# Optimization experiments

Hardware: AMD Instinct MI355X
Metric: run time of the kernel (lower is better)

## Reference

```python
import jax, jax.numpy as jnp
import numpy as np

B, TE, TD, E, H, V, A, MAXOOV = 8, 400, 100, 128, 256, 50000, 612, 50
VEXT = V + MAXOOV


def setup_inputs():
    key = jax.random.key(0)
    it = iter(jax.random.split(key, 40))
    def nrm(shape, s=0.05):
        return jax.random.normal(next(it), shape, jnp.float32) * s
    inp = {
        "encoder_tokens": jax.random.randint(next(it), (B, TE), 0, V, dtype=jnp.int32),
        "decoder_tokens": jax.random.randint(next(it), (B, TD), 0, V, dtype=jnp.int32),
        "encoder_ext_tokens": jax.random.randint(next(it), (B, TE), 0, VEXT, dtype=jnp.int32),
        "encoder_mask": jnp.ones((B, TE), jnp.float32),
        "embedding": nrm((V, E)),
        "Wih_f": nrm((E, 4 * H)), "Whh_f": nrm((H, 4 * H)), "b_f": jnp.zeros((4 * H,), jnp.float32),
        "Wih_b": nrm((E, 4 * H)), "Whh_b": nrm((H, 4 * H)), "b_b": jnp.zeros((4 * H,), jnp.float32),
        "Wred": nrm((2 * H, H)), "bred": jnp.zeros((H,), jnp.float32),
        "Wenc_feat": nrm((2 * H, A)), "benc_feat": jnp.zeros((A,), jnp.float32),
        "v": nrm((A,), 1.0),
        "Wx": nrm((E + 2 * H, E)), "bx": jnp.zeros((E,), jnp.float32),
        "Wih_d": nrm((E, 4 * H)), "Whh_d": nrm((H, 4 * H)), "b_d": jnp.zeros((4 * H,), jnp.float32),
        "Wdf": nrm((TD, 2 * H, A)), "bdf": jnp.zeros((TD, A), jnp.float32),
        "Wpg": nrm((2 * H + H + H + E, 1)), "bpg": jnp.zeros((1,), jnp.float32),
        "Wout": nrm((H + 2 * H, H)), "bout": jnp.zeros((H,), jnp.float32),
        "Wv": nrm((H, V)), "bv": jnp.zeros((V,), jnp.float32),
    }
    return inp


def _lstm(xs, Wih, Whh, b):
    # xs: [T, B, E] -> outputs [T, B, H], final (h, c)
    def step(carry, x):
        h, c = carry
        g = x @ Wih + h @ Whh + b
        i, f, gg, o = jnp.split(g, 4, axis=-1)  # torch gate order i,f,g,o
        c = jax.nn.sigmoid(f) * c + jax.nn.sigmoid(i) * jnp.tanh(gg)
        h = jax.nn.sigmoid(o) * jnp.tanh(c)
        return (h, c), h
    z = jnp.zeros((xs.shape[1], Whh.shape[0]), xs.dtype)
    (hT, cT), hs = jax.lax.scan(step, (z, z), xs)
    return hs, hT, cT


def reference(encoder_tokens, decoder_tokens, encoder_ext_tokens, encoder_mask,
              embedding, Wih_f, Whh_f, b_f, Wih_b, Whh_b, b_b, Wred, bred,
              Wenc_feat, benc_feat, v, Wx, bx, Wih_d, Whh_d, b_d, Wdf, bdf,
              Wpg, bpg, Wout, bout, Wv, bv):
    # ---- bidirectional LSTM encoder (full-length sequences, mask == 1) ----
    enc_emb = embedding[encoder_tokens]               # [B, TE, E]
    xs = enc_emb.transpose(1, 0, 2)                   # [TE, B, E]
    hf, hTf, cTf = _lstm(xs, Wih_f, Whh_f, b_f)
    hb_rev, hTb, cTb = _lstm(xs[::-1], Wih_b, Whh_b, b_b)
    hb = hb_rev[::-1]
    enc_out = jnp.concatenate([hf, hb], -1).transpose(1, 0, 2)  # [B, TE, 2H]

    # ---- state reducer (original uses reduce_h_layer for BOTH h and c) ----
    h0 = jax.nn.relu(jnp.concatenate([hTf, hTb], -1) @ Wred + bred)
    c0 = jax.nn.relu(jnp.concatenate([cTf, cTb], -1) @ Wred + bred)

    # ---- 1x1 conv == linear on encoder states ----
    enc_feat = enc_out @ Wenc_feat + benc_feat        # [B, TE, A]

    dec_emb = embedding[decoder_tokens].transpose(1, 0, 2)  # [TD, B, E]

    def dec_step(carry, xs_t):
        h, c, ctx = carry
        emb_t, Wdf_t, bdf_t = xs_t
        x = jnp.concatenate([emb_t, ctx], -1) @ Wx + bx          # [B, E]
        g = x @ Wih_d + h @ Whh_d + b_d
        i, f, gg, o = jnp.split(g, 4, axis=-1)
        c = jax.nn.sigmoid(f) * c + jax.nn.sigmoid(i) * jnp.tanh(gg)
        h = jax.nn.sigmoid(o) * jnp.tanh(c)
        dec_feat = jnp.concatenate([h, c], -1) @ Wdf_t + bdf_t   # [B, A] (per-step weights)
        e = jnp.einsum('a,bta->bt', v, jnp.tanh(enc_feat + dec_feat[:, None, :]))
        attn = jax.nn.softmax(e, axis=-1) * encoder_mask
        attn = attn / attn.sum(-1, keepdims=True)
        ctx = jnp.einsum('bt,btd->bd', attn, enc_out)            # [B, 2H]
        p_gen = jax.nn.sigmoid(jnp.concatenate([ctx, h, c, x], -1) @ Wpg + bpg)  # [B, 1]
        out = jnp.concatenate([h, ctx], -1) @ Wout + bout        # [B, H]
        return (h, c, ctx), (out, attn, p_gen)

    ctx0 = jnp.zeros((enc_out.shape[0], 2 * H), enc_out.dtype)
    _, (outs, attns, pgens) = jax.lax.scan(dec_step, (h0, c0, ctx0), (dec_emb, Wdf, bdf))
    # outs [TD,B,H], attns [TD,B,TE], pgens [TD,B,1]

    # ---- pointer-generator mixture over extended vocab ----
    vocab_dist = jax.nn.softmax(outs @ Wv + bv, axis=-1)         # [TD, B, V]
    vocab_dist = pgens * vocab_dist
    attn_w = (1.0 - pgens) * attns                               # [TD, B, TE]

    def scatter_one(a, idx):
        return jnp.zeros((VEXT,), a.dtype).at[idx].add(a)
    copy_dist = jax.vmap(jax.vmap(scatter_one, in_axes=(0, 0)), in_axes=(0, None))(
        attn_w, encoder_ext_tokens)                              # [TD, B, VEXT]

    extra = jnp.zeros(vocab_dist.shape[:2] + (MAXOOV,), vocab_dist.dtype)
    final = jnp.concatenate([vocab_dist, extra], -1) + copy_dist # [TD, B, VEXT]
    return final
```

## Files before the change

### kernel.cpp

```cpp
#include <hip/hip_runtime.h>

#define DEVI __device__ __forceinline__

constexpr int B_ = 8, TE_ = 400, TD_ = 100, E_ = 128, H_ = 256;
constexpr int A_ = 612, V_ = 50000, VEXT_ = 50050;
constexpr int H4_ = 1024, H2_ = 512;
constexpr int NS_ = 16, SLW_ = 40;

constexpr size_t OFS_HBF  = 0;
constexpr size_t OFS_HBB  = 4096;
constexpr size_t OFS_CT   = 8192;
constexpr size_t OFS_CHC  = 12288;
constexpr size_t OFS_PG   = 32896;
constexpr size_t OFS_SROW = 33696;
constexpr size_t OFS_FLG  = 34496;
constexpr size_t OFS_ATT  = 35520;
constexpr size_t OFS_EO   = 355520;
constexpr size_t OFS_OUTS = OFS_EO;
constexpr size_t OFS_EF   = OFS_EO + (size_t)B_*TE_*H2_;

constexpr size_t DO_GDEC = 2ull*(size_t)TE_*B_*H4_;
constexpr size_t DO_XPRE = DO_GDEC + (size_t)TD_*B_*H4_;
constexpr size_t DO_CTXH = DO_XPRE + (size_t)TD_*B_*E_;
constexpr size_t DO_HCH  = DO_CTXH + (size_t)TD_*B_*H2_;
constexpr size_t DO_WCG  = DO_HCH + (size_t)TD_*B_*H2_;
constexpr size_t DO_EOWT = DO_WCG + (size_t)H2_*H4_;
constexpr size_t DO_EPB  = DO_EOWT + (size_t)B_*H4_*TE_;

#if defined(__has_builtin)
#if __has_builtin(__builtin_amdgcn_rcpf)
#define HAS_RCPF 1
#endif
#endif

DEVI float rcp_fast(float x) {
#ifdef HAS_RCPF
  return __builtin_amdgcn_rcpf(x);
#else
  return 1.0f / x;
#endif
}

DEVI float sigm(float x) { return rcp_fast(1.0f + __expf(-x)); }
DEVI float tanh_fast(float x) {
  float e = __expf(2.0f * x);
  return 1.0f - 2.0f * rcp_fast(e + 1.0f);
}

DEVI float ld_at(const float* p) {
  unsigned u = __hip_atomic_load((const unsigned*)p, __ATOMIC_RELAXED, __HIP_MEMORY_SCOPE_AGENT);
  return __uint_as_float(u);
}
DEVI void st_at(float* p, float v) {
  __hip_atomic_store((unsigned*)p, __float_as_uint(v), __ATOMIC_RELAXED, __HIP_MEMORY_SCOPE_AGENT);
}

#define WAIT_VM() do { asm volatile("s_waitcnt vmcnt(0)" ::: "memory"); \
                       __builtin_amdgcn_sched_barrier(0); } while (0)

DEVI float wave_max(float v) {
#pragma unroll
  for (int o = 32; o; o >>= 1) v = fmaxf(v, __shfl_xor(v, o));
  return v;
}
DEVI float wave_sum(float v) {
#pragma unroll
  for (int o = 32; o; o >>= 1) v += __shfl_xor(v, o);
  return v;
}

DEVI void flag_bar(unsigned* flags, int ncheck, int slot, unsigned ep, int stride) {
  __syncthreads();
  if (threadIdx.x == 0) {
    asm volatile("s_waitcnt vmcnt(0)" ::: "memory");
    __hip_atomic_store(&flags[slot * stride], ep, __ATOMIC_RELAXED, __HIP_MEMORY_SCOPE_AGENT);
  }
  if ((int)threadIdx.x < ncheck) {
    while (__hip_atomic_load(&flags[threadIdx.x * stride], __ATOMIC_RELAXED,
                             __HIP_MEMORY_SCOPE_AGENT) < ep) {
      __builtin_amdgcn_s_sleep(2);
    }
  }
  __syncthreads();
  asm volatile("" ::: "memory");
}

__global__ __launch_bounds__(256) void k0_wcg(
    const float* __restrict__ Wx, const float* __restrict__ Wih_d,
    float* __restrict__ dob, float* __restrict__ ws)
{
  __shared__ float AsT[32 * 64];
  __shared__ float Bsh[32 * 64];
  const float* Am = Wx + 128 * 128;
  float* C = dob + DO_WCG;
  const int ct = blockIdx.x, rt = blockIdx.y, tid = threadIdx.x;
  if (ct == 0 && rt == 0) {
    for (int i = tid; i < 8192; i += 256) ws[OFS_HBF + i] = 0.0f;
    unsigned* f = (unsigned*)(ws + OFS_FLG);
    for (int i = tid; i < 1024; i += 256) f[i] = 0u;
  }
  const int c0 = ct * 64, r0 = rt * 64;
  const int tx = tid & 15, ty = tid >> 4;
  float4 acc0 = make_float4(0,0,0,0), acc1 = acc0, acc2 = acc0, acc3 = acc0;
  for (int kc = 0; kc < 4; ++kc) {
#pragma unroll
    for (int i = 0; i < 2; ++i) {
      int q = tid * 2 + i;
      int r = q >> 3, kq = q & 7;
      float4 v = *(const float4*)&Am[(size_t)(r0 + r) * 128 + kc * 32 + kq * 4];
      AsT[(kq * 4 + 0) * 64 + r] = v.x; AsT[(kq * 4 + 1) * 64 + r] = v.y;
      AsT[(kq * 4 + 2) * 64 + r] = v.z; AsT[(kq * 4 + 3) * 64 + r] = v.w;
    }
#pragma unroll
    for (int i = 0; i < 2; ++i) {
      int q = tid * 2 + i;
      int kk = q >> 4, cq = q & 15;
      *(float4*)&Bsh[kk * 64 + cq * 4] =
          *(const float4*)&Wih_d[(size_t)(kc * 32 + kk) * H4_ + c0 + cq * 4];
    }
    __syncthreads();
#pragma unroll
    for (int kk = 0; kk < 32; ++kk) {
      float4 w4 = *(float4*)&Bsh[kk * 64 + tx * 4];
      const float* ar = &AsT[kk * 64 + ty * 4];
      acc0.x += ar[0]*w4.x; acc0.y += ar[0]*w4.y; acc0.z += ar[0]*w4.z; acc0.w += ar[0]*w4.w;
      acc1.x += ar[1]*w4.x; acc1.y += ar[1]*w4.y; acc1.z += ar[1]*w4.z; acc1.w += ar[1]*w4.w;
      acc2.x += ar[2]*w4.x; acc2.y += ar[2]*w4.y; acc2.z += ar[2]*w4.z; acc2.w += ar[2]*w4.w;
      acc3.x += ar[3]*w4.x; acc3.y += ar[3]*w4.y; acc3.z += ar[3]*w4.z; acc3.w += ar[3]*w4.w;
    }
    __syncthreads();
  }
  float4 r4[4] = {acc0, acc1, acc2, acc3};
#pragma unroll
  for (int i = 0; i < 4; ++i)
    *(float4*)&C[(size_t)(r0 + ty * 4 + i) * H4_ + c0 + tx * 4] = r4[i];
}

__global__ __launch_bounds__(256) void k1d_dec_pre(
    const int* __restrict__ dtok, const float* __restrict__ emb,
    const float* __restrict__ Wx, const float* __restrict__ bx,
    const float* __restrict__ Wih_d, const float* __restrict__ b_d,
    float* __restrict__ dob)
{
  __shared__ float er[8 * 128];
  __shared__ float xl[8 * 128];
  const int t = blockIdx.x, tid = threadIdx.x;
  for (int i = tid; i < 1024; i += 256) {
    int b = i >> 7, e = i & 127;
    er[i] = emb[(size_t)dtok[b * TD_ + t] * E_ + e];
  }
  __syncthreads();
  {
    const int col = tid & 127, bh = tid >> 7;
#pragma unroll
    for (int ii = 0; ii < 4; ++ii) {
      int b = bh + (ii << 1);
      float acc = bx[col];
      for (int k = 0; k < 128; ++k) acc += er[b * 128 + k] * Wx[(size_t)k * E_ + col];
      xl[b * 128 + col] = acc;
      dob[DO_XPRE + ((size_t)t * 8 + b) * E_ + col] = acc;
    }
  }
  __syncthreads();
  float bv[4];
#pragma unroll
  for (int g = 0; g < 4; ++g) bv[g] = b_d[g * H_ + tid];
  float af[32];
#pragma unroll
  for (int i = 0; i < 32; ++i) af[i] = bv[i & 3];
  for (int e = 0; e < E_; ++e) {
    float w[4];
#pragma unroll
    for (int g = 0; g < 4; ++g) w[g] = Wih_d[(size_t)e * H4_ + g * H_ + tid];
#pragma unroll
    for (int b = 0; b < 8; ++b) {
      float x = xl[b * 128 + e];
#pragma unroll
      for (int g = 0; g < 4; ++g) af[b * 4 + g] += x * w[g];
    }
  }
#pragma unroll
  for (int b = 0; b < 8; ++b)
#pragma unroll
    for (int g = 0; g < 4; ++g)
      dob[DO_GDEC + ((size_t)t * 8 + b) * H4_ + g * H_ + tid] = af[b * 4 + g];
}

__global__ __launch_bounds__(256, 1) void k2_encoder_scan(
    const int* __restrict__ etok, const float* __restrict__ emb,
    const float* __restrict__ Wih_f, const float* __restrict__ b_f,
    const float* __restrict__ Wih_b, const float* __restrict__ b_b,
    const float* __restrict__ Whh_f, const float* __restrict__ Whh_b,
    float* __restrict__ ws)
{
  __shared__ float sm[3072];
  __shared__ float part[2048];
  __shared__ int tokL[B_ * TE_];
  const int bid = blockIdx.x, tid = threadIdx.x;
  const int dir = bid >> 5, c0 = (bid & 31) * 8;
  const float* Whh = dir ? Whh_b : Whh_f;
  const float* Wih = dir ? Wih_b : Wih_f;
  const float* bbp = dir ? b_b : b_f;
  float* hb = ws + (dir ? OFS_HBB : OFS_HBF);
  float* cT = ws + OFS_CT;
  float* eo = ws + OFS_EO;
  unsigned* flg = (unsigned*)(ws + OFS_FLG) + (dir ? 128 : 0);
  const int slot = bid & 31;

  for (int i = tid; i < B_ * TE_; i += 256) tokL[i] = etok[i];

  const int jl = tid >> 3, kg = tid & 7;
  const int gt = jl >> 3, hcl = jl & 7;
  const int jcol = gt * H_ + c0 + hcl;
  float wreg[48];
#pragma unroll
  for (int kk = 0; kk < 48; ++kk) {
    if (kk < 32) wreg[kk] = Whh[(size_t)(kg + kk * 8) * H4_ + jcol];
    else         wreg[kk] = Wih[(size_t)(kg + (kk - 32) * 8) * H4_ + jcol];
  }
  const int uhc = tid >> 3, ub = tid & 7;
  float bias[4] = {0, 0, 0, 0};
  if (tid < 64) {
#pragma unroll
    for (int g = 0; g < 4; ++g) bias[g] = bbp[g * H_ + c0 + uhc];
  }
  const int ebb = tid >> 5, e4 = tid & 31;
  float c_reg = 0.0f;
  unsigned ep = 0;
  __syncthreads();

  for (int t = 0; t < TE_; ++t) {
    const int te = dir ? (TE_ - 1 - t) : t;
    float* hrd = hb + (t & 1) * 2048;
    float* hwr = hb + ((t & 1) ^ 1) * 2048;
    float4 ev = *(const float4*)&emb[(size_t)tokL[ebb * TE_ + te] * E_ + e4 * 4];
    float4 v0, v1;
    const float* a0p = &hrd[tid * 8];
    const float* a1p = &hrd[tid * 8 + 4];
    asm volatile(
        "global_load_dwordx4 %0, %2, off sc0 sc1\n\t"
        "global_load_dwordx4 %1, %3, off sc0 sc1"
        : "=&v"(v0), "=&v"(v1) : "v"(a0p), "v"(a1p));
    WAIT_VM();
    *(float4*)&sm[tid * 8] = v0;
    *(float4*)&sm[tid * 8 + 4] = v1;
    *(float4*)&sm[2048 + ebb * 128 + e4 * 4] = ev;
    __syncthreads();
    float acc[8] = {0, 0, 0, 0, 0, 0, 0, 0};
#pragma unroll
    for (int kk = 0; kk < 32; ++kk) {
      float w = wreg[kk];
      const float* hp = &sm[(kg + kk * 8) * 8];
#pragma unroll
      for (int b = 0; b < 8; ++b) acc[b] += hp[b] * w;
    }
#pragma unroll
    for (int kk = 32; kk < 48; ++kk) {
      float w = wreg[kk];
      const int e = kg + (kk - 32) * 8;
#pragma unroll
      for (int b = 0; b < 8; ++b) acc[b] += sm[2048 + b * 128 + e] * w;
    }
    *(float4*)&part[(jl * 8 + kg) * 8]     = make_float4(acc[0], acc[1], acc[2], acc[3]);
    *(float4*)&part[(jl * 8 + kg) * 8 + 4] = make_float4(acc[4], acc[5], acc[6], acc[7]);
    __syncthreads();
    if (tid < 64) {
      float g[4];
#pragma unroll
      for (int gg = 0; gg < 4; ++gg) {
        float s = bias[gg];
#pragma unroll
        for (int k2 = 0; k2 < 8; ++k2) s += part[((gg * 8 + uhc) * 8 + k2) * 8 + ub];
        g[gg] = s;
      }
      float ci = sigm(g[0]), cf = sigm(g[1]), cg = tanh_fast(g[2]), co = sigm(g[3]);
      c_reg = cf * c_reg + ci * cg;
      float hn = co * tanh_fast(c_reg);
      st_at(&hwr[(c0 + uhc) * 8 + ub], hn);
      eo[((size_t)ub * TE_ + te) * H2_ + dir * H_ + c0 + uhc] = hn;
      if (t == TE_ - 1) cT[ub * H2_ + dir * H_ + c0 + uhc] = c_reg;
    }
    ep++; flag_bar(flg, 32, slot, ep, 4);
  }
}

__global__ __launch_bounds__(256) void k3_encfeat(
    const float* __restrict__ eo, const float* __restrict__ Wef,
    const float* __restrict__ bef, float* __restrict__ ef)
{
  __shared__ float AsT[32 * 64];
  __shared__ float Wsh[32 * 64];
  const int ct = blockIdx.x, rt = blockIdx.y, tid = threadIdx.x;
  const int c0 = ct * 64, r0 = rt * 64;
  const int tx = tid & 15, ty = tid >> 4;
  float4 acc0 = make_float4(0,0,0,0), acc1 = acc0, acc2 = acc0, acc3 = acc0;
  for (int kc = 0; kc < 16; ++kc) {
#pragma unroll
    for (int i = 0; i < 2; ++i) {
      int q = tid * 2 + i;
      int r = q >> 3, kq = q & 7;
      float4 v = *(const float4*)&eo[(size_t)(r0 + r) * H2_ + kc * 32 + kq * 4];
      AsT[(kq * 4 + 0) * 64 + r] = v.x; AsT[(kq * 4 + 1) * 64 + r] = v.y;
      AsT[(kq * 4 + 2) * 64 + r] = v.z; AsT[(kq * 4 + 3) * 64 + r] = v.w;
    }
#pragma unroll
    for (int i = 0; i < 2; ++i) {
      int q = tid * 2 + i;
      int kk = q >> 4, cq = q & 15;
      int col = c0 + cq * 4;
      float4 v = make_float4(0,0,0,0);
      if (col < A_) v = *(const float4*)&Wef[(size_t)(kc * 32 + kk) * A_ + col];
      *(float4*)&Wsh[kk * 64 + cq * 4] = v;
    }
    __syncthreads();
#pragma unroll
    for (int kk = 0; kk < 32; ++kk) {
      float4 w4 = *(float4*)&Wsh[kk * 64 + tx * 4];
      const float* ar = &AsT[kk * 64 + ty * 4];
      acc0.x += ar[0]*w4.x; acc0.y += ar[0]*w4.y; acc0.z += ar[0]*w4.z; acc0.w += ar[0]*w4.w;
      acc1.x += ar[1]*w4.x; acc1.y += ar[1]*w4.y; acc1.z += ar[1]*w4.z; acc1.w += ar[1]*w4.w;
      acc2.x += ar[2]*w4.x; acc2.y += ar[2]*w4.y; acc2.z += ar[2]*w4.z; acc2.w += ar[2]*w4.w;
      acc3.x += ar[3]*w4.x; acc3.y += ar[3]*w4.y; acc3.z += ar[3]*w4.z; acc3.w += ar[3]*w4.w;
    }
    __syncthreads();
  }
  const int col = c0 + tx * 4;
  if (col < A_) {
    float4 bb = *(const float4*)&bef[col];
    float4 r4[4] = {acc0, acc1, acc2, acc3};
#pragma unroll
    for (int i = 0; i < 4; ++i) {
      int row = r0 + ty * 4 + i;
      float4 o = make_float4(r4[i].x + bb.x, r4[i].y + bb.y, r4[i].z + bb.z, r4[i].w + bb.w);
      *(float4*)&ef[(size_t)row * A_ + col] = o;
    }
  }
}

__global__ __launch_bounds__(256) void k3b_eowt(
    const float* __restrict__ eo, const float* __restrict__ dob_c, float* __restrict__ dob)
{
  __shared__ float Wt[32 * 64];
  __shared__ float Et[32 * 40];
  const float* Wcg = dob_c + DO_WCG;
  float* eoWT = dob + DO_EOWT;
  const int jt = blockIdx.x, tt = blockIdx.y, b = blockIdx.z, tid = threadIdx.x;
  const int j0 = jt * 64, te0 = tt * 40;
  const int j_l = tid & 63, tq = tid >> 6;
  float acc[10];
#pragma unroll
  for (int u = 0; u < 10; ++u) acc[u] = 0.0f;
  for (int kc = 0; kc < 16; ++kc) {
#pragma unroll
    for (int i = 0; i < 2; ++i) {
      int q = tid * 2 + i;
      int kk = q >> 4, j4 = q & 15;
      *(float4*)&Wt[kk * 64 + j4 * 4] =
          *(const float4*)&Wcg[(size_t)(kc * 32 + kk) * H4_ + j0 + j4 * 4];
    }
#pragma unroll
    for (int i = 0; i < 2; ++i) {
      int q = tid + i * 256;
      if (q < 320) {
        int te_l = q >> 3, kq = q & 7;
        float4 v = *(const float4*)&eo[((size_t)b * TE_ + te0 + te_l) * H2_ + kc * 32 + kq * 4];
        Et[(kq * 4 + 0) * 40 + te_l] = v.x; Et[(kq * 4 + 1) * 40 + te_l] = v.y;
        Et[(kq * 4 + 2) * 40 + te_l] = v.z; Et[(kq * 4 + 3) * 40 + te_l] = v.w;
      }
    }
    __syncthreads();
#pragma unroll
    for (int kk = 0; kk < 32; ++kk) {
      float w = Wt[kk * 64 + j_l];
      const float* ep2 = &Et[kk * 40 + tq * 10];
#pragma unroll
      for (int u = 0; u < 10; ++u) acc[u] += w * ep2[u];
    }
    __syncthreads();
  }
  float* outp = &eoWT[((size_t)b * H4_ + j0 + j_l) * TE_ + te0 + tq * 10];
#pragma unroll
  for (int u = 0; u < 10; ++u) outp[u] = acc[u];
}

__global__ __launch_bounds__(512, 1) void k4_decoder(
    const float* __restrict__ maskp,
    const float* __restrict__ Wred, const float* __restrict__ bred,
    const float* __restrict__ Whh_d,
    const float* __restrict__ Wdf, const float* __restrict__ bdf,
    const float* __restrict__ vvec, float* __restrict__ ws, float* __restrict__ dob)
{
  __shared__ float eoW[TE_ * 64];
  __shared__ float eu[TE_];
  __shared__ float hcL[512];
  __shared__ float red[16];
  __shared__ float gdL[64];
  __shared__ float gl[64];
  __shared__ float pgl[64 * 9];
  __shared__ float prt[1280];
  __shared__ float dfl[48];
  __shared__ float bdfL[48];
  __shared__ float vvL[48];

  float* chc = ws + OFS_CHC;
  float* att = ws + OFS_ATT;
  const float* efG = ws + OFS_EF;
  const float* hbf = ws + OFS_HBF;
  const float* hbb = ws + OFS_HBB;
  const float* cT  = ws + OFS_CT;
  unsigned* flgF = (unsigned*)(ws + OFS_FLG) + 256;
  const float* gdec = dob + DO_GDEC;
  const float* eoWT = dob + DO_EOWT;
  float* epb = dob + DO_EPB;
  float* hch = dob + DO_HCH;
  const int bid = blockIdx.x, tid = threadIdx.x;
  const int b = bid >> 4, s = bid & 15;
  unsigned* flgG = (unsigned*)(ws + OFS_FLG) + 512 + b * 64;
  const int a0 = s * SLW_, w = (s == 15) ? 12 : SLW_;
  const int nq = w >> 2;

  for (int i = tid; i < 64 * 100; i += 512) {
    int jgi = i / 100, c = i - jgi * 100;
    int jreal = (jgi >> 4) * 256 + s * 16 + (jgi & 15);
    float4 v = *(const float4*)&eoWT[((size_t)b * H4_ + jreal) * TE_ + c * 4];
    eoW[(c * 4 + 0) * 64 + jgi] = v.x;
    eoW[(c * 4 + 1) * 64 + jgi] = v.y;
    eoW[(c * 4 + 2) * 64 + jgi] = v.z;
    eoW[(c * 4 + 3) * 64 + jgi] = v.w;
  }
  const int jg = tid & 63, l8 = tid >> 6;
  const int jreal = (jg >> 4) * 256 + s * 16 + (jg & 15);
  float wreg[32];
#pragma unroll
  for (int kk = 0; kk < 32; ++kk)
    wreg[kk] = Whh_d[(size_t)(l8 + kk * 8) * H4_ + jreal];
  if (tid < w) vvL[tid] = vvec[a0 + tid];

  if (bid < 32) {
    const int isC = bid >> 4, pb = (bid >> 1) & 7, half = bid & 1;
    if (tid < 512)
      hcL[tid] = isC ? cT[pb * H2_ + tid]
                     : (tid < H_ ? hbf[tid * 8 + pb] : hbb[(tid - H_) * 8 + pb]);
    __syncthreads();
    {
      const int col_l = tid & 127, ks = tid >> 7;
      float acc = 0.0f;
      for (int kk = 0; kk < 128; ++kk) {
        int k = ks * 128 + kk;
        acc += hcL[k] * Wred[(size_t)k * H_ + half * 128 + col_l];
      }
      prt[ks * 128 + col_l] = acc;
    }
    __syncthreads();
    if (tid < 128) {
      float v2 = fmaxf(prt[tid] + prt[128 + tid] + prt[256 + tid] + prt[384 + tid] +
                       bred[half * 128 + tid], 0.0f);
      st_at(&chc[pb * H2_ + isC * H_ + half * 128 + tid], v2);
    }
  } else {
    float dm = 0.0f;
#pragma unroll
    for (int i = 0; i < 7; ++i) {
      int f = (bid - 32) * 3264 + i * 512 + tid;
      if (i * 512 + tid < 3264 && f < H2_ * A_) dm += Wdf[f];
    }
    asm volatile("" :: "v"(dm));
  }
  unsigned ep = 1;
  flag_bar(flgF, 128, bid, ep, 2);

  float c_reg = 0.0f;
  if (tid < 16) c_reg = ld_at(&chc[b * H2_ + H_ + s * 16 + tid]);
  unsigned epg = 0;

  for (int t = 0; t <= TD_; ++t) {
    const int cur = t & 1, nxt = cur ^ 1;

    {
      const int teA = (tid < TE_) ? tid : TE_ - 1;
      const int tcl = (t < TD_) ? t : TD_ - 1;
      const float* ae = &epb[((size_t)b * TE_ + teA) * 16];
      const float* ah = &chc[cur * 4096 + b * H2_ + (tid & 63) * 4];
      const int gi = tid & 15;
      const float* agd = &gdec[((size_t)tcl * 8 + b) * H4_ +
                               (gi >> 2) * 256 + s * 16 + (gi & 3) * 4];
      float4 v0, v1, v2, v3, vh, vgd;
      asm volatile(
          "global_load_dwordx4 %0, %6, off sc0 sc1\n\t"
          "global_load_dwordx4 %1, %7, off sc0 sc1\n\t"
          "global_load_dwordx4 %2, %8, off sc0 sc1\n\t"
          "global_load_dwordx4 %3, %9, off sc0 sc1\n\t"
          "global_load_dwordx4 %4, %10, off sc0 sc1\n\t"
          "global_load_dwordx4 %5, %11, off sc0 sc1"
          : "=&v"(v0), "=&v"(v1), "=&v"(v2), "=&v"(v3), "=&v"(vh), "=&v"(vgd)
          : "v"(ae), "v"(ae + 4), "v"(ae + 8), "v"(ae + 12), "v"(ah), "v"(agd));
      WAIT_VM();
      if (t > 0 && tid < TE_)
        eu[tid] = (v0.x + v0.y + v0.z + v0.w) + (v1.x + v1.y + v1.z + v1.w) +
                  (v2.x + v2.y + v2.z + v2.w) + (v3.x + v3.y + v3.z + v3.w);
      if (tid < 64) *(float4*)&hcL[tid * 4] = vh;
      if (tid < 16) *(float4*)&gdL[(gi >> 2) * 16 + (gi & 3) * 4] = vgd;
      __syncthreads();

      float inv = 0.0f;
      if (t > 0) {
        float m = (tid < TE_) ? eu[tid] : -3.4e38f;
        m = wave_max(m);
        if ((tid & 63) == 0) red[tid >> 6] = m;
        __syncthreads();
        m = red[0];
#pragma unroll
        for (int i = 1; i < 8; ++i) m = fmaxf(m, red[i]);
        float u = 0.0f;
        if (tid < TE_) {
          u = __expf(eu[tid] - m) * maskp[b * TE_ + tid];
          eu[tid] = u;
        }
        float sl = wave_sum(u);
        if ((tid & 63) == 0) red[8 + (tid >> 6)] = sl;
        __syncthreads();
        float S = 0.0f;
#pragma unroll
        for (int i = 0; i < 8; ++i) S += red[8 + i];
        inv = rcp_fast(S);
      }

      if (t > 0 && tid < 25)
        att[((size_t)(t - 1) * 8 + b) * TE_ + s * 25 + tid] = eu[s * 25 + tid] * inv;

      if (t < TD_) {
        float accG = 0.0f, accW = 0.0f;
        if (t > 0) {
          for (int te = l8; te < TE_; te += 8)
            accG += eoW[te * 64 + jg] * eu[te];
        }
#pragma unroll
        for (int kk = 0; kk < 32; ++kk)
          accW += wreg[kk] * hcL[l8 + kk * 8];
        pgl[jg * 9 + l8] = accG * inv + accW;
        __syncthreads();
        if (tid < 64) {
          float sg = gdL[tid];
#pragma unroll
          for (int l = 0; l < 8; ++l) sg += pgl[tid * 9 + l];
          gl[tid] = sg;
        }
        __syncthreads();
        if (tid < 16) {
          float g0 = gl[tid], g1 = gl[16 + tid], g2 = gl[32 + tid], g3 = gl[48 + tid];
          float ci = sigm(g0), cf = sigm(g1), cg = tanh_fast(g2), co = sigm(g3);
          c_reg = cf * c_reg + ci * cg;
          float hn = co * tanh_fast(c_reg);
          int hc = s * 16 + tid;
          st_at(&chc[nxt * 4096 + b * H2_ + hc], hn);
          st_at(&chc[nxt * 4096 + b * H2_ + H_ + hc], c_reg);
          hch[((size_t)t * 8 + b) * H2_ + hc] = hn;
          hch[((size_t)t * 8 + b) * H2_ + H_ + hc] = c_reg;
        }
      }
    }
    if (t == TD_) break;
    epg++; flag_bar(flgG, 16, s, epg, 4);

    {
      {
        const float* ahc = &chc[nxt * 4096 + b * H2_ + (tid & 127) * 4];
        const int cl = (tid < 10) ? tid : 9;
        const float* abf = &bdf[(size_t)t * A_ + a0 + cl * 4];
        float4 vhc, vbf;
        asm volatile(
            "global_load_dwordx4 %0, %2, off sc0 sc1\n\t"
            "global_load_dwordx4 %1, %3, off sc0 sc1"
            : "=&v"(vhc), "=&v"(vbf) : "v"(ahc), "v"(abf));
        WAIT_VM();
        if (tid < 128) *(float4*)&hcL[tid * 4] = vhc;
        if (tid < 10) *(float4*)&bdfL[tid * 4] = vbf;
      }
      __syncthreads();

      const float* wp = Wdf + (size_t)t * H2_ * A_;
      {
        const int kq = tid >> 4, al = tid & 15;
        if (al < nq) {
          float4 a4 = make_float4(0, 0, 0, 0);
          const float* wpc = wp + a0 + al * 4;
#pragma unroll
          for (int i = 0; i < 16; ++i) {
            int k = kq * 16 + i;
            float4 w4 = *(const float4*)&wpc[(size_t)k * A_];
            float hv = hcL[k];
            a4.x += hv * w4.x; a4.y += hv * w4.y; a4.z += hv * w4.z; a4.w += hv * w4.w;
          }
          *(float4*)&prt[(kq * 10 + al) * 4] = a4;
        }
      }
      float dm = 0.0f;
      if (t + 1 < TD_) {
        const float* wp1 = Wdf + (size_t)(t + 1) * H2_ * A_;
#pragma unroll
        for (int q = 0; q < 2; ++q) {
          int f = tid + q * 512;
          if (f < 640) {
            int r = f / 10, c4 = f - r * 10;
            if (c4 < nq) {
              float4 vx = *(const float4*)&wp1[(size_t)(b * 64 + r) * A_ + a0 + c4 * 4];
              dm += vx.x + vx.y + vx.z + vx.w;
            }
          }
        }
      }
      __syncthreads();
      if (tid < w) {
        float ssum = bdfL[tid];
        const int c4 = tid >> 2, r = tid & 3;
#pragma unroll
        for (int kq = 0; kq < 32; ++kq) ssum += prt[(kq * 10 + c4) * 4 + r];
        dfl[tid] = ssum;
      }
      __syncthreads();

      if (tid < TE_) {
        const float* efp = &efG[((size_t)b * TE_ + tid) * A_ + a0];
        float acc = 0.0f;
        for (int q = 0; q < nq; ++q) {
          float4 e4 = *(const float4*)&efp[q * 4];
          const float* dd = &dfl[q * 4];
          const float* vv = &vvL[q * 4];
          acc += vv[0] * tanh_fast(e4.x + dd[0]);
          acc += vv[1] * tanh_fast(e4.y + dd[1]);
          acc += vv[2] * tanh_fast(e4.z + dd[2]);
          acc += vv[3] * tanh_fast(e4.w + dd[3]);
        }
        st_at(&epb[((size_t)b * TE_ + tid) * 16 + s], acc);
      }
      asm volatile("" :: "v"(dm));
    }
    epg++; flag_bar(flgG, 16, s, epg, 4);
  }
}

__global__ __launch_bounds__(256) void k4c_ctx(
    const float* __restrict__ ws, float* __restrict__ dob)
{
  __shared__ float AsT[32 * 64];
  __shared__ float Bsh[32 * 64];
  const float* att = ws + OFS_ATT;
  const float* eo  = ws + OFS_EO;
  float* ctxh = dob + DO_CTXH;
  const int ct = blockIdx.x, rt = blockIdx.y, b = blockIdx.z, tid = threadIdx.x;
  const int c0 = ct * 64, r0 = rt * 64;
  const int tx = tid & 15, ty = tid >> 4;
  float4 acc0 = make_float4(0,0,0,0), acc1 = acc0, acc2 = acc0, acc3 = acc0;
  for (int kc = 0; kc < 13; ++kc) {
#pragma unroll
    for (int i = 0; i < 2; ++i) {
      int q = tid * 2 + i;
      int r = q >> 3, kq = q & 7;
      int k = kc * 32 + kq * 4;
      float4 v = make_float4(0, 0, 0, 0);
      if (k < TE_ && r0 + r < TD_)
        v = *(const float4*)&att[((size_t)(r0 + r) * 8 + b) * TE_ + k];
      AsT[(kq * 4 + 0) * 64 + r] = v.x; AsT[(kq * 4 + 1) * 64 + r] = v.y;
      AsT[(kq * 4 + 2) * 64 + r] = v.z; AsT[(kq * 4 + 3) * 64 + r] = v.w;
    }
#pragma unroll
    for (int i = 0; i < 2; ++i) {
      int q = tid * 2 + i;
      int kk = q >> 4, cq = q & 15;
      int k = kc * 32 + kk;
      float4 v = make_float4(0, 0, 0, 0);
      if (k < TE_) v = *(const float4*)&eo[((size_t)b * TE_ + k) * H2_ + c0 + cq * 4];
      *(float4*)&Bsh[kk * 64 + cq * 4] = v;
    }
    __syncthreads();
#pragma unroll
    for (int kk = 0; kk < 32; ++kk) {
      float4 w4 = *(float4*)&Bsh[kk * 64 + tx * 4];
      const float* ar = &AsT[kk * 64 + ty * 4];
      acc0.x += ar[0]*w4.x; acc0.y += ar[0]*w4.y; acc0.z += ar[0]*w4.z; acc0.w += ar[0]*w4.w;
      acc1.x += ar[1]*w4.x; acc1.y += ar[1]*w4.y; acc1.z += ar[1]*w4.z; acc1.w += ar[1]*w4.w;
      acc2.x += ar[2]*w4.x; acc2.y += ar[2]*w4.y; acc2.z += ar[2]*w4.z; acc2.w += ar[2]*w4.w;
      acc3.x += ar[3]*w4.x; acc3.y += ar[3]*w4.y; acc3.z += ar[3]*w4.z; acc3.w += ar[3]*w4.w;
    }
    __syncthreads();
  }
  float4 r4[4] = {acc0, acc1, acc2, acc3};
#pragma unroll
  for (int i = 0; i < 4; ++i) {
    int row = r0 + ty * 4 + i;
    if (row < TD_)
      *(float4*)&ctxh[((size_t)row * 8 + b) * H2_ + c0 + tx * 4] = r4[i];
  }
}

__global__ __launch_bounds__(256) void k4b_post(
    const float* __restrict__ Wx, const float* __restrict__ Wout, const float* __restrict__ bout,
    const float* __restrict__ Wpg, const float* __restrict__ bpg,
    float* __restrict__ ws, const float* __restrict__ dob)
{
  __shared__ float hcl[4096], ctxl[4096], cpl[4096], xl[1024], red2[256];
  const int t = blockIdx.x, tid = threadIdx.x;
  const float* hch  = dob + DO_HCH;
  const float* ctxh = dob + DO_CTXH;
  const float* xpre = dob + DO_XPRE;
  for (int i = tid; i < 4096; i += 256) {
    hcl[i]  = hch[(size_t)t * 4096 + i];
    ctxl[i] = ctxh[(size_t)t * 4096 + i];
    cpl[i]  = t ? ctxh[(size_t)(t - 1) * 4096 + i] : 0.0f;
  }
  __syncthreads();
  {
    const int col = tid & 127, bh = tid >> 7;
#pragma unroll
    for (int ii = 0; ii < 4; ++ii) {
      int b = bh + (ii << 1);
      float acc = xpre[(size_t)t * 1024 + b * E_ + col];
      for (int k = 0; k < H2_; ++k) acc += cpl[b * H2_ + k] * Wx[(size_t)(128 + k) * E_ + col];
      xl[b * E_ + col] = acc;
    }
  }
  __syncthreads();
  {
    const int col = tid;
    for (int b = 0; b < 8; ++b) {
      float acc = bout[col];
      for (int k = 0; k < 768; ++k)
        acc += (k < H_ ? hcl[b * H2_ + k] : ctxl[b * H2_ + (k - H_)]) * Wout[(size_t)k * H_ + col];
      ws[OFS_OUTS + ((size_t)t * 8 + b) * H_ + col] = acc;
    }
  }
  {
    const int b = tid >> 5, sg = tid & 31;
    float acc = 0.0f;
    for (int j = 0; j < 36; ++j) {
      int k = sg * 36 + j;
      float xv;
      if (k < H2_)       xv = ctxl[b * H2_ + k];
      else if (k < 768)  xv = hcl[b * H2_ + (k - H2_)];
      else if (k < 1024) xv = hcl[b * H2_ + H_ + (k - 768)];
      else               xv = xl[b * E_ + (k - 1024)];
      acc += xv * Wpg[k];
    }
    red2[tid] = acc;
    __syncthreads();
    if (tid < 8) {
      float s = 0.0f;
      for (int k2 = 0; k2 < 32; ++k2) s += red2[tid * 32 + k2];
      ws[OFS_PG + t * 8 + tid] = sigm(s + bpg[0]);
    }
  }
}

__global__ __launch_bounds__(256) void k5a_logits(
    const float* __restrict__ outs, const float* __restrict__ Wv,
    const float* __restrict__ bv, float* __restrict__ out)
{
  __shared__ float aT[32 * 64];
  __shared__ float wl[32 * 256];
  const int rt = blockIdx.x, ct = blockIdx.y, tid = threadIdx.x;
  const int r0 = rt * 64, c0 = ct * 256;
  const int cq = tid & 63, rg = tid >> 6;
  float4 acc[16];
#pragma unroll
  for (int i = 0; i < 16; ++i) acc[i] = make_float4(0, 0, 0, 0);
  for (int kc = 0; kc < 8; ++kc) {
#pragma unroll
    for (int i = 0; i < 2; ++i) {
      int q = tid * 2 + i;
      int r = q >> 3, kq = q & 7;
      float4 v = make_float4(0, 0, 0, 0);
      if (r0 + r < 800) v = *(const float4*)&outs[(size_t)(r0 + r) * H_ + kc * 32 + kq * 4];
      aT[(kq * 4 + 0) * 64 + r] = v.x; aT[(kq * 4 + 1) * 64 + r] = v.y;
      aT[(kq * 4 + 2) * 64 + r] = v.z; aT[(kq * 4 + 3) * 64 + r] = v.w;
    }
#pragma unroll
    for (int i = 0; i < 8; ++i) {
      int q = tid + i * 256;
      int kk = q >> 6, c4 = q & 63;
      int col = c0 + c4 * 4;
      float4 v = make_float4(0, 0, 0, 0);
      if (col < V_) v = *(const float4*)&Wv[(size_t)(kc * 32 + kk) * V_ + col];
      *(float4*)&wl[kk * 256 + c4 * 4] = v;
    }
    __syncthreads();
#pragma unroll
    for (int kk = 0; kk < 32; ++kk) {
      float4 w4 = *(float4*)&wl[kk * 256 + cq * 4];
      const float* ar = &aT[kk * 64 + rg * 16];
#pragma unroll
      for (int rr = 0; rr < 16; ++rr) {
        float a = ar[rr];
        acc[rr].x += a * w4.x; acc[rr].y += a * w4.y;
        acc[rr].z += a * w4.z; acc[rr].w += a * w4.w;
      }
    }
    __syncthreads();
  }
  const int col = c0 + cq * 4;
  if (col < V_) {
    float4 bb = *(const float4*)&bv[col];
#pragma unroll
    for (int rr = 0; rr < 16; ++rr) {
      int row = r0 + rg * 16 + rr;
      if (row < 800) {
        float2 lo = make_float2(acc[rr].x + bb.x, acc[rr].y + bb.y);
        float2 hi = make_float2(acc[rr].z + bb.z, acc[rr].w + bb.w);
        *(float2*)&out[(size_t)row * VEXT_ + col] = lo;
        *(float2*)&out[(size_t)row * VEXT_ + col + 2] = hi;
      }
    }
  }
}

__global__ __launch_bounds__(256) void k5b_rowsum(const float* __restrict__ out, float* __restrict__ Srow)
{
  __shared__ float red[256];
  const int r = blockIdx.x, tid = threadIdx.x;
  const float* base = out + (size_t)r * VEXT_;
  float s = 0.0f;
  for (int i = tid; i < V_ / 2; i += 256) {
    float2 v = *(const float2*)&base[i * 2];
    s += __expf(v.x) + __expf(v.y);
  }
  red[tid] = s; __syncthreads();
  for (int st = 128; st > 0; st >>= 1) { if (tid < st) red[tid] += red[tid + st]; __syncthreads(); }
  if (tid == 0) Srow[r] = red[0];
}

__global__ __launch_bounds__(256) void k5c_final(
    float* __restrict__ out, const float* __restrict__ Srow, const float* __restrict__ pg)
{
  const int cc = blockIdx.x, r = blockIdx.y, tid = threadIdx.x;
  const float scale = pg[r] * rcp_fast(Srow[r]);
  float* base = out + (size_t)r * VEXT_;
#pragma unroll
  for (int i = 0; i < 4; ++i) {
    int col = cc * 2048 + i * 512 + tid * 2;
    if (col < V_) {
      float2 v = *(float2*)&base[col];
      v.x = __expf(v.x) * scale; v.y = __expf(v.y) * scale;
      *(float2*)&base[col] = v;
    } else if (col < VEXT_) {
      *(float2*)&base[col] = make_float2(0.0f, 0.0f);
    }
  }
}

__global__ __launch_bounds__(256) void k5d_scatter(
    float* __restrict__ out, const float* __restrict__ ws, const int* __restrict__ ext)
{
  const int r = blockIdx.x, tid = threadIdx.x;
  const int b = r & 7;
  const float* at = ws + OFS_ATT + (size_t)r * TE_;
  const float w = 1.0f - ws[OFS_PG + r];
  float* base = out + (size_t)r * VEXT_;
  for (int i = tid; i < TE_; i += 256)
    atomicAdd(&base[ext[b * TE_ + i]], w * at[i]);
}

extern "C" void kernel_launch(void* const* d_in, const int* in_sizes, int n_in,
                              void* d_out, int out_size, void* d_ws, size_t ws_size,
                              hipStream_t stream) {
  const int*   etok  = (const int*)d_in[0];
  const int*   dtok  = (const int*)d_in[1];
  const int*   ext   = (const int*)d_in[2];
  const float* maskp = (const float*)d_in[3];
  const float* emb   = (const float*)d_in[4];
  const float* Wih_f = (const float*)d_in[5];
  const float* Whh_f = (const float*)d_in[6];
  const float* b_f   = (const float*)d_in[7];
  const float* Wih_b = (const float*)d_in[8];
  const float* Whh_b = (const float*)d_in[9];
  const float* b_b   = (const float*)d_in[10];
  const float* Wred  = (const float*)d_in[11];
  const float* bred  = (const float*)d_in[12];
  const float* Wef   = (const float*)d_in[13];
  const float* bef   = (const float*)d_in[14];
  const float* vvec  = (const float*)d_in[15];
  const float* Wx    = (const float*)d_in[16];
  const float* bx    = (const float*)d_in[17];
  const float* Wih_d = (const float*)d_in[18];
  const float* Whh_d = (const float*)d_in[19];
  const float* b_d   = (const float*)d_in[20];
  const float* Wdf   = (const float*)d_in[21];
  const float* bdf   = (const float*)d_in[22];
  const float* Wpg   = (const float*)d_in[23];
  const float* bpg   = (const float*)d_in[24];
  const float* Wout  = (const float*)d_in[25];
  const float* bout  = (const float*)d_in[26];
  const float* Wv    = (const float*)d_in[27];
  const float* bv    = (const float*)d_in[28];
  float* out = (float*)d_out;
  float* wsf = (float*)d_ws;
  float* dob = out;

  k0_wcg<<<dim3(16, 8), 256, 0, stream>>>(Wx, Wih_d, dob, wsf);
  k1d_dec_pre<<<100, 256, 0, stream>>>(dtok, emb, Wx, bx, Wih_d, b_d, dob);

  {
    void* args2[9] = {(void*)&etok, (void*)&emb, (void*)&Wih_f, (void*)&b_f,
                      (void*)&Wih_b, (void*)&b_b, (void*)&Whh_f, (void*)&Whh_b, (void*)&wsf};
    if (hipLaunchCooperativeKernel((void*)k2_encoder_scan, dim3(64), dim3(256), args2, 0, stream) != hipSuccess)
      k2_encoder_scan<<<64, 256, 0, stream>>>(etok, emb, Wih_f, b_f, Wih_b, b_b, Whh_f, Whh_b, wsf);
  }

  k3_encfeat<<<dim3(10, 50), 256, 0, stream>>>(wsf + OFS_EO, Wef, bef, wsf + OFS_EF);
  k3b_eowt<<<dim3(16, 10, 8), 256, 0, stream>>>(wsf + OFS_EO, dob, dob);

  {
    void* args4[9] = {(void*)&maskp, (void*)&Wred, (void*)&bred, (void*)&Whh_d,
                      (void*)&Wdf, (void*)&bdf, (void*)&vvec, (void*)&wsf, (void*)&dob};
    if (hipLaunchCooperativeKernel((void*)k4_decoder, dim3(128), dim3(512), args4, 0, stream) != hipSuccess)
      k4_decoder<<<128, 512, 0, stream>>>(maskp, Wred, bred, Whh_d, Wdf, bdf, vvec, wsf, dob);
  }

  k4c_ctx<<<dim3(8, 2, 8), 256, 0, stream>>>(wsf, dob);
  k4b_post<<<100, 256, 0, stream>>>(Wx, Wout, bout, Wpg, bpg, wsf, dob);

  k5a_logits<<<dim3(13, 196), 256, 0, stream>>>(wsf + OFS_OUTS, Wv, bv, out);
  k5b_rowsum<<<800, 256, 0, stream>>>(out, wsf + OFS_SROW);
  k5c_final<<<dim3(25, 800), 256, 0, stream>>>(out, wsf + OFS_SROW, wsf + OFS_PG);
  k5d_scatter<<<800, 256, 0, stream>>>(out, wsf, ext);
}
```

Before: 3.734 ms.

## Replace flag barriers with tagged 64-bit value polling in recurrent scans

Cross-block flag barriers in the encoder and decoder scan kernels are replaced by packing each published float with a step tag into a 64-bit atomic word. Consumers spin on exactly the values they need until the tags match. This removes the global barrier round-trip (store flag, poll all peers, syncthreads) per timestep and lets producers and consumers synchronise point-to-point. The cost is doubled storage and traffic for the shared state buffers, plus relaxed-ordering correctness that depends on the tag scheme and on reinitialisation.

```diff
diff --git a/kernel.cpp b/kernel.cpp
--- a/kernel.cpp
+++ b/kernel.cpp
@@ -1,6 +1,7 @@
 #include <hip/hip_runtime.h>
 
 #define DEVI __device__ __forceinline__
+typedef unsigned long long u64;
 
 constexpr int B_ = 8, TE_ = 400, TD_ = 100, E_ = 128, H_ = 256;
 constexpr int A_ = 612, V_ = 50000, VEXT_ = 50050;
@@ -8,14 +9,14 @@
 constexpr int NS_ = 16, SLW_ = 40;
 
 constexpr size_t OFS_HBF  = 0;
-constexpr size_t OFS_HBB  = 4096;
-constexpr size_t OFS_CT   = 8192;
-constexpr size_t OFS_CHC  = 12288;
-constexpr size_t OFS_PG   = 32896;
-constexpr size_t OFS_SROW = 33696;
-constexpr size_t OFS_FLG  = 34496;
-constexpr size_t OFS_ATT  = 35520;
-constexpr size_t OFS_EO   = 355520;
+constexpr size_t OFS_HBB  = 8192;
+constexpr size_t OFS_CT   = 16384;
+constexpr size_t OFS_CHC  = 20480;
+constexpr size_t OFS_PG   = 36864;
+constexpr size_t OFS_SROW = 37664;
+constexpr size_t OFS_FLG  = 38464;
+constexpr size_t OFS_ATT  = 39488;
+constexpr size_t OFS_EO   = 359488;
 constexpr size_t OFS_OUTS = OFS_EO;
 constexpr size_t OFS_EF   = OFS_EO + (size_t)B_*TE_*H2_;
 
@@ -51,12 +52,17 @@
   unsigned u = __hip_atomic_load((const unsigned*)p, __ATOMIC_RELAXED, __HIP_MEMORY_SCOPE_AGENT);
   return __uint_as_float(u);
 }
-DEVI void st_at(float* p, float v) {
-  __hip_atomic_store((unsigned*)p, __float_as_uint(v), __ATOMIC_RELAXED, __HIP_MEMORY_SCOPE_AGENT);
-}
-
-#define WAIT_VM() do { asm volatile("s_waitcnt vmcnt(0)" ::: "memory"); \
-                       __builtin_amdgcn_sched_barrier(0); } while (0)
+DEVI u64 ld64_at(const u64* p) {
+  return __hip_atomic_load(p, __ATOMIC_RELAXED, __HIP_MEMORY_SCOPE_AGENT);
+}
+DEVI void st64_at(u64* p, u64 v) {
+  __hip_atomic_store(p, v, __ATOMIC_RELAXED, __HIP_MEMORY_SCOPE_AGENT);
+}
+DEVI u64 packft(float f, unsigned tag) {
+  return (u64)__float_as_uint(f) | ((u64)tag << 32);
+}
+DEVI float lowf(u64 v) { return __uint_as_float((unsigned)v); }
+DEVI unsigned hitag(u64 v) { return (unsigned)(v >> 32); }
 
 DEVI float wave_max(float v) {
 #pragma unroll
@@ -95,7 +101,7 @@
   float* C = dob + DO_WCG;
   const int ct = blockIdx.x, rt = blockIdx.y, tid = threadIdx.x;
   if (ct == 0 && rt == 0) {
-    for (int i = tid; i < 8192; i += 256) ws[OFS_HBF + i] = 0.0f;
+    for (int i = tid; i < 16384; i += 256) ws[OFS_HBF + i] = 0.0f;
     unsigned* f = (unsigned*)(ws + OFS_FLG);
     for (int i = tid; i < 1024; i += 256) f[i] = 0u;
   }
@@ -201,11 +207,9 @@
   const float* Whh = dir ? Whh_b : Whh_f;
   const float* Wih = dir ? Wih_b : Wih_f;
   const float* bbp = dir ? b_b : b_f;
-  float* hb = ws + (dir ? OFS_HBB : OFS_HBF);
+  u64* hb = (u64*)(ws + (dir ? OFS_HBB : OFS_HBF));
   float* cT = ws + OFS_CT;
   float* eo = ws + OFS_EO;
-  unsigned* flg = (unsigned*)(ws + OFS_FLG) + (dir ? 128 : 0);
-  const int slot = bid & 31;
 
   for (int i = tid; i < B_ * TE_; i += 256) tokL[i] = etok[i];
 
@@ -226,24 +230,27 @@
   }
   const int ebb = tid >> 5, e4 = tid & 31;
   float c_reg = 0.0f;
-  unsigned ep = 0;
   __syncthreads();
 
   for (int t = 0; t < TE_; ++t) {
     const int te = dir ? (TE_ - 1 - t) : t;
-    float* hrd = hb + (t & 1) * 2048;
-    float* hwr = hb + ((t & 1) ^ 1) * 2048;
     float4 ev = *(const float4*)&emb[(size_t)tokL[ebb * TE_ + te] * E_ + e4 * 4];
-    float4 v0, v1;
-    const float* a0p = &hrd[tid * 8];
-    const float* a1p = &hrd[tid * 8 + 4];
-    asm volatile(
-        "global_load_dwordx4 %0, %2, off sc0 sc1\n\t"
-        "global_load_dwordx4 %1, %3, off sc0 sc1"
-        : "=&v"(v0), "=&v"(v1) : "v"(a0p), "v"(a1p));
-    WAIT_VM();
-    *(float4*)&sm[tid * 8] = v0;
-    *(float4*)&sm[tid * 8 + 4] = v1;
+    {
+      const u64* src = hb + (size_t)(t & 1) * 2048 + tid * 8;
+      const unsigned want = (unsigned)t;
+      u64 v[8];
+      bool ok;
+      do {
+#pragma unroll
+        for (int i = 0; i < 8; ++i) v[i] = ld64_at(src + i);
+        ok = true;
+#pragma unroll
+        for (int i = 0; i < 8; ++i) ok &= (hitag(v[i]) == want);
+        if (!ok) __builtin_amdgcn_s_sleep(1);
+      } while (!ok);
+#pragma unroll
+      for (int i = 0; i < 8; ++i) sm[tid * 8 + i] = lowf(v[i]);
+    }
     *(float4*)&sm[2048 + ebb * 128 + e4 * 4] = ev;
     __syncthreads();
     float acc[8] = {0, 0, 0, 0, 0, 0, 0, 0};
@@ -276,11 +283,11 @@
       float ci = sigm(g[0]), cf = sigm(g[1]), cg = tanh_fast(g[2]), co = sigm(g[3]);
       c_reg = cf * c_reg + ci * cg;
       float hn = co * tanh_fast(c_reg);
-      st_at(&hwr[(c0 + uhc) * 8 + ub], hn);
+      st64_at(&hb[(size_t)((t & 1) ^ 1) * 2048 + (c0 + uhc) * 8 + ub],
+              packft(hn, (unsigned)(t + 1)));
       eo[((size_t)ub * TE_ + te) * H2_ + dir * H_ + c0 + uhc] = hn;
       if (t == TE_ - 1) cT[ub * H2_ + dir * H_ + c0 + uhc] = c_reg;
     }
-    ep++; flag_bar(flg, 32, slot, ep, 4);
   }
 }
 
@@ -402,20 +409,19 @@
   __shared__ float bdfL[48];
   __shared__ float vvL[48];
 
-  float* chc = ws + OFS_CHC;
+  u64* chcU = (u64*)(ws + OFS_CHC);
   float* att = ws + OFS_ATT;
   const float* efG = ws + OFS_EF;
-  const float* hbf = ws + OFS_HBF;
-  const float* hbb = ws + OFS_HBB;
+  const u64* hbfU = (const u64*)(ws + OFS_HBF);
+  const u64* hbbU = (const u64*)(ws + OFS_HBB);
   const float* cT  = ws + OFS_CT;
   unsigned* flgF = (unsigned*)(ws + OFS_FLG) + 256;
   const float* gdec = dob + DO_GDEC;
   const float* eoWT = dob + DO_EOWT;
-  float* epb = dob + DO_EPB;
+  u64* epbU = (u64*)(dob + DO_EPB);
   float* hch = dob + DO_HCH;
   const int bid = blockIdx.x, tid = threadIdx.x;
   const int b = bid >> 4, s = bid & 15;
-  unsigned* flgG = (unsigned*)(ws + OFS_FLG) + 512 + b * 64;
   const int a0 = s * SLW_, w = (s == 15) ? 12 : SLW_;
   const int nq = w >> 2;
 
@@ -436,11 +442,14 @@
     wreg[kk] = Whh_d[(size_t)(l8 + kk * 8) * H4_ + jreal];
   if (tid < w) vvL[tid] = vvec[a0 + tid];
 
+  if (tid < TE_) st64_at(&epbU[((size_t)b * TE_ + tid) * 16 + s], 0ULL);
+  if (bid >= 32 && bid < 40) st64_at(&chcU[4096 + (bid - 32) * 512 + tid], 0ULL);
   if (bid < 32) {
     const int isC = bid >> 4, pb = (bid >> 1) & 7, half = bid & 1;
     if (tid < 512)
       hcL[tid] = isC ? cT[pb * H2_ + tid]
-                     : (tid < H_ ? hbf[tid * 8 + pb] : hbb[(tid - H_) * 8 + pb]);
+                     : (tid < H_ ? lowf(ld64_at(hbfU + (size_t)tid * 8 + pb))
+                                 : lowf(ld64_at(hbbU + (size_t)(tid - H_) * 8 + pb)));
     __syncthreads();
     {
       const int col_l = tid & 127, ks = tid >> 7;
@@ -455,7 +464,7 @@
     if (tid < 128) {
       float v2 = fmaxf(prt[tid] + prt[128 + tid] + prt[256 + tid] + prt[384 + tid] +
                        bred[half * 128 + tid], 0.0f);
-      st_at(&chc[pb * H2_ + isC * H_ + half * 128 + tid], v2);
+      st64_at(&chcU[(size_t)pb * 512 + isC * 256 + half * 128 + tid], packft(v2, 0u));
     }
   } else {
     float dm = 0.0f;
@@ -466,40 +475,55 @@
     }
     asm volatile("" :: "v"(dm));
   }
-  unsigned ep = 1;
-  flag_bar(flgF, 128, bid, ep, 2);
+  flag_bar(flgF, 128, bid, 1, 2);
 
   float c_reg = 0.0f;
-  if (tid < 16) c_reg = ld_at(&chc[b * H2_ + H_ + s * 16 + tid]);
-  unsigned epg = 0;
+  if (tid < 16) c_reg = lowf(ld64_at(&chcU[(size_t)b * 512 + 256 + s * 16 + tid]));
 
   for (int t = 0; t <= TD_; ++t) {
-    const int cur = t & 1, nxt = cur ^ 1;
 
     {
-      const int teA = (tid < TE_) ? tid : TE_ - 1;
-      const int tcl = (t < TD_) ? t : TD_ - 1;
-      const float* ae = &epb[((size_t)b * TE_ + teA) * 16];
-      const float* ah = &chc[cur * 4096 + b * H2_ + (tid & 63) * 4];
-      const int gi = tid & 15;
-      const float* agd = &gdec[((size_t)tcl * 8 + b) * H4_ +
-                               (gi >> 2) * 256 + s * 16 + (gi & 3) * 4];
-      float4 v0, v1, v2, v3, vh, vgd;
-      asm volatile(
-          "global_load_dwordx4 %0, %6, off sc0 sc1\n\t"
-          "global_load_dwordx4 %1, %7, off sc0 sc1\n\t"
-          "global_load_dwordx4 %2, %8, off sc0 sc1\n\t"
-          "global_load_dwordx4 %3, %9, off sc0 sc1\n\t"
-          "global_load_dwordx4 %4, %10, off sc0 sc1\n\t"
-          "global_load_dwordx4 %5, %11, off sc0 sc1"
-          : "=&v"(v0), "=&v"(v1), "=&v"(v2), "=&v"(v3), "=&v"(vh), "=&v"(vgd)
-          : "v"(ae), "v"(ae + 4), "v"(ae + 8), "v"(ae + 12), "v"(ah), "v"(agd));
-      WAIT_VM();
-      if (t > 0 && tid < TE_)
-        eu[tid] = (v0.x + v0.y + v0.z + v0.w) + (v1.x + v1.y + v1.z + v1.w) +
-                  (v2.x + v2.y + v2.z + v2.w) + (v3.x + v3.y + v3.z + v3.w);
-      if (tid < 64) *(float4*)&hcL[tid * 4] = vh;
-      if (tid < 16) *(float4*)&gdL[(gi >> 2) * 16 + (gi & 3) * 4] = vgd;
+      if (t > 0 && tid < TE_) {
+        const u64* src = epbU + ((size_t)b * TE_ + tid) * 16;
+        const unsigned want = (unsigned)t;
+        u64 v[16];
+        bool ok;
+        do {
+#pragma unroll
+          for (int i = 0; i < 16; ++i) v[i] = ld64_at(src + i);
+          ok = true;
+#pragma unroll
+          for (int i = 0; i < 16; ++i) ok &= (hitag(v[i]) == want);
+          if (!ok) __builtin_amdgcn_s_sleep(1);
+        } while (!ok);
+        float sum = 0.0f;
+#pragma unroll
+        for (int i = 0; i < 16; ++i) sum += lowf(v[i]);
+        eu[tid] = sum;
+      }
+      if (t < TD_ && tid >= 400 && tid < 464) {
+        const int u = tid - 400;
+        const u64* src = chcU + (size_t)(t & 1) * 4096 + b * 512 + u * 4;
+        const unsigned want = (unsigned)t;
+        u64 v[4];
+        bool ok;
+        do {
+#pragma unroll
+          for (int i = 0; i < 4; ++i) v[i] = ld64_at(src + i);
+          ok = true;
+#pragma unroll
+          for (int i = 0; i < 4; ++i) ok &= (hitag(v[i]) == want);
+          if (!ok) __builtin_amdgcn_s_sleep(1);
+        } while (!ok);
+#pragma unroll
+        for (int i = 0; i < 4; ++i) hcL[u * 4 + i] = lowf(v[i]);
+      }
+      if (t < TD_ && tid >= 464 && tid < 480) {
+        const int gi = tid - 464;
+        float4 vgd = *(const float4*)&gdec[((size_t)t * 8 + b) * H4_ +
+                                           (gi >> 2) * 256 + s * 16 + (gi & 3) * 4];
+        *(float4*)&gdL[(gi >> 2) * 16 + (gi & 3) * 4] = vgd;
+      }
       __syncthreads();
 
       float inv = 0.0f;
@@ -552,29 +576,37 @@
           c_reg = cf * c_reg + ci * cg;
           float hn = co * tanh_fast(c_reg);
           int hc = s * 16 + tid;
-          st_at(&chc[nxt * 4096 + b * H2_ + hc], hn);
-          st_at(&chc[nxt * 4096 + b * H2_ + H_ + hc], c_reg);
+          u64* dst = chcU + (size_t)((t + 1) & 1) * 4096 + b * 512;
+          st64_at(&dst[hc], packft(hn, (unsigned)(t + 1)));
+          st64_at(&dst[H_ + hc], packft(c_reg, (unsigned)(t + 1)));
           hch[((size_t)t * 8 + b) * H2_ + hc] = hn;
           hch[((size_t)t * 8 + b) * H2_ + H_ + hc] = c_reg;
         }
       }
     }
     if (t == TD_) break;
-    epg++; flag_bar(flgG, 16, s, epg, 4);
 
     {
+      if (tid < 128) {
+        const u64* src = chcU + (size_t)((t + 1) & 1) * 4096 + b * 512 + tid * 4;
+        const unsigned want = (unsigned)(t + 1);
+        u64 v[4];
+        bool ok;
+        do {
+#pragma unroll
+          for (int i = 0; i < 4; ++i) v[i] = ld64_at(src + i);
+          ok = true;
+#pragma unroll
+          for (int i = 0; i < 4; ++i) ok &= (hitag(v[i]) == want);
+          if (!ok) __builtin_amdgcn_s_sleep(1);
+        } while (!ok);
+#pragma unroll
+        for (int i = 0; i < 4; ++i) hcL[tid * 4 + i] = lowf(v[i]);
+      }
       {
-        const float* ahc = &chc[nxt * 4096 + b * H2_ + (tid & 127) * 4];
-        const int cl = (tid < 10) ? tid : 9;
-        const float* abf = &bdf[(size_t)t * A_ + a0 + cl * 4];
-        float4 vhc, vbf;
-        asm volatile(
-            "global_load_dwordx4 %0, %2, off sc0 sc1\n\t"
-            "global_load_dwordx4 %1, %3, off sc0 sc1"
-            : "=&v"(vhc), "=&v"(vbf) : "v"(ahc), "v"(abf));
-        WAIT_VM();
-        if (tid < 128) *(float4*)&hcL[tid * 4] = vhc;
-        if (tid < 10) *(float4*)&bdfL[tid * 4] = vbf;
+        const int maxc = (w + 3) >> 2;
+        if (tid < maxc)
+          *(float4*)&bdfL[tid * 4] = *(const float4*)&bdf[(size_t)t * A_ + a0 + tid * 4];
       }
       __syncthreads();
 
@@ -631,11 +663,10 @@
           acc += vv[2] * tanh_fast(e4.z + dd[2]);
           acc += vv[3] * tanh_fast(e4.w + dd[3]);
         }
-        st_at(&epb[((size_t)b * TE_ + tid) * 16 + s], acc);
+        st64_at(&epbU[((size_t)b * TE_ + tid) * 16 + s], packft(acc, (unsigned)(t + 1)));
       }
       asm volatile("" :: "v"(dm));
     }
-    epg++; flag_bar(flgG, 16, s, epg, 4);
   }
 }
 
```

New measurement: 5.336 ms. +42.9%, slower.
